# Performance work log

Measured on AMD Instinct MI355X. Metric: run time of the kernel, lower is better.

## Reference

```python
import jax, jax.numpy as jnp
import numpy as np

B, C, H = 128, 3, 224
PATCH_NUM, PS = 14, 16          # patch_size = image_size / patch_num
NP = PATCH_NUM * PATCH_NUM      # 196 patches
TOP_K = 20
D = 768                         # ViT-B hidden dim
NUM_CLASSES = 1000


def setup_inputs() -> dict:
    key = jax.random.key(0)
    k1, k2, k3, k4, k5 = jax.random.split(key, 5)
    return {
        "inputs": jax.random.normal(k1, (B, C, H, H), jnp.float32),
        "patch_grad": jax.random.normal(k2, (B, NP, D), jnp.float32),
        "attack_w": jax.random.uniform(k3, (C, H, H), jnp.float32),  # torch.rand init
        "w_cls": jax.random.normal(k4, (C * NP, NUM_CLASSES), jnp.float32) * 0.02,
        "targets": jax.random.randint(k5, (B,), 0, NUM_CLASSES),
    }


def reference(inputs, patch_grad, attack_w, w_cls, targets):
    # --- top-k patch selection from patch-embedding gradients ---
    # sum over batch, then over embedding dim -> [NP]
    sum_patch = patch_grad.sum(axis=0).sum(axis=1)
    _, top_idx = jax.lax.top_k(sum_patch, TOP_K)  # distinct patch indices

    # --- vectorized equivalent of the per-pixel double loop ---
    # patch (ix, iy) -> pixel block [ix*PS:(ix+1)*PS, iy*PS:(iy+1)*PS]
    ix = top_idx // PATCH_NUM
    iy = top_idx % PATCH_NUM
    mask_p = jnp.zeros((PATCH_NUM, PATCH_NUM), inputs.dtype).at[ix, iy].set(1.0)
    mask = jnp.kron(mask_p, jnp.ones((PS, PS), inputs.dtype))  # [H, H] pixel mask
    x = inputs + mask[None, None, :, :] * attack_w[None, :, :, :]  # [B,C,H,H]

    # --- surrogate classifier head (stand-in for aux_vit second forward) ---
    # per-patch average pool, flatten, linear -> logits [B, NUM_CLASSES]
    pooled = x.reshape(B, C, PATCH_NUM, PS, PATCH_NUM, PS).mean(axis=(3, 5))
    logits = pooled.reshape(B, -1) @ w_cls

    targets_prob = jax.nn.softmax(logits, axis=1)
    # original applies CrossEntropyLoss to the *probabilities* (treats them as logits)
    logp = jax.nn.log_softmax(targets_prob, axis=1)
    ce = -jnp.take_along_axis(logp, targets[:, None], axis=1)[:, 0]  # [B]

    u = 0.0
    l2loss = jnp.mean(attack_w * attack_w)
    loss = u * l2loss - (1.0 - u) * ce.mean()
    return targets_prob, loss
```

## Files before the change

kernel.cpp:

```cpp
#include <hip/hip_runtime.h>
#include <math.h>

#define PA_OFF    0
#define APOOL_OFF 2048
#define MA_OFF    3072
#define IPOOL_OFF 4096
#define PL_OFF    81920

__global__ __launch_bounds__(256) void k1_fused(
    const float* __restrict__ inputs,
    const float* __restrict__ patch_grad,
    const float* __restrict__ attack_w,
    float* __restrict__ ws)
{
  __shared__ __align__(16) float lds[448];
  const int bid = blockIdx.x;
  const int t   = threadIdx.x;

  if (bid < 2688) {
    const int img = bid / 7, pp = bid - img * 7;
    const float* src = inputs + (size_t)img * 50176 + (size_t)pp * 32 * 224;
    if (t < 224) {
      const int c4 = t % 56, rg = t / 56;
      float4 v[8];
      #pragma unroll
      for (int j = 0; j < 8; ++j) {
        const int row = (j >> 2) * 16 + (j & 3) * 4 + rg;
        v[j] = *(const float4*)(src + row * 224 + c4 * 4);
      }
      float s0 = 0.f, s1 = 0.f;
      #pragma unroll
      for (int j = 0; j < 4; ++j) s0 += (v[j].x + v[j].y) + (v[j].z + v[j].w);
      #pragma unroll
      for (int j = 4; j < 8; ++j) s1 += (v[j].x + v[j].y) + (v[j].z + v[j].w);
      lds[(0 * 4 + rg) * 56 + c4] = s0;
      lds[(1 * 4 + rg) * 56 + c4] = s1;
    }
    __syncthreads();
    if (t < 28) {
      const int pxl = t / 14, py = t - pxl * 14;
      float s = 0.f;
      #pragma unroll
      for (int rg = 0; rg < 4; ++rg)
        #pragma unroll
        for (int i4 = 0; i4 < 4; ++i4)
          s += lds[(pxl * 4 + rg) * 56 + py * 4 + i4];
      const int b = img / 3, c = img - b * 3;
      const int px = pp * 2 + pxl;
      ws[IPOOL_OFF + (size_t)b * 588 + c * 196 + px * 14 + py] = s * (1.f / 256.f);
    }
  } else if (bid < 4256) {
    const int a = bid - 2688;
    const int p = a >> 3, chunk = a & 7;
    const float* base = patch_grad + (size_t)chunk * 16 * 150528 + (size_t)p * 768;
    float4 v[12];
    #pragma unroll
    for (int j = 0; j < 12; ++j) {
      const int idx = j * 256 + t;
      const int r   = idx / 192;
      const int off = idx - r * 192;
      v[j] = *(const float4*)(base + (size_t)r * 150528 + off * 4);
    }
    float acc = 0.f;
    #pragma unroll
    for (int j = 0; j < 12; ++j) acc += (v[j].x + v[j].y) + (v[j].z + v[j].w);
    #pragma unroll
    for (int o = 32; o > 0; o >>= 1) acc += __shfl_down(acc, o, 64);
    if ((t & 63) == 0) lds[t >> 6] = acc;
    __syncthreads();
    if (t == 0) ws[PA_OFF + a] = lds[0] + lds[1] + lds[2] + lds[3];
  } else {
    const int a = bid - 4256;
    const int c = a / 14, px = a - c * 14;
    const float* img = attack_w + (size_t)c * 50176;
    if (t < 224) {
      const int c4 = t % 56, rg = t / 56;
      float4 v[4];
      #pragma unroll
      for (int jj = 0; jj < 4; ++jj) {
        const int row = px * 16 + jj * 4 + rg;
        v[jj] = *(const float4*)(img + row * 224 + c4 * 4);
      }
      float s = 0.f;
      #pragma unroll
      for (int jj = 0; jj < 4; ++jj) s += (v[jj].x + v[jj].y) + (v[jj].z + v[jj].w);
      lds[rg * 56 + c4] = s;
    }
    __syncthreads();
    if (t < 14) {
      float s = 0.f;
      #pragma unroll
      for (int rg = 0; rg < 4; ++rg)
        for (int i4 = 0; i4 < 4; ++i4)
          s += lds[rg * 56 + t * 4 + i4];
      ws[APOOL_OFF + c * 196 + px * 14 + t] = s * (1.f / 256.f);
    }
  }
}

__global__ __launch_bounds__(256) void k2_topk(float* __restrict__ ws,
                                               float* __restrict__ d_loss)
{
  __shared__ float sp[196];
  __shared__ float maskp[196];
  const int t = threadIdx.x;
  if (t < 196) {
    const float* pa = ws + PA_OFF;
    float s = 0.f;
    #pragma unroll
    for (int j = 0; j < 8; ++j) s += pa[t * 8 + j];
    sp[t] = s;
  }
  if (t == 0) *d_loss = 0.f;
  __syncthreads();
  if (t < 196) {
    const float v = sp[t];
    int cnt = 0;
    for (int j = 0; j < 196; ++j) {
      const float u = sp[j];
      cnt += (u > v || (u == v && j < t)) ? 1 : 0;
    }
    maskp[t] = (cnt < 20) ? 1.f : 0.f;
  }
  __syncthreads();
  for (int k = t; k < 588; k += 256) {
    const int p = k % 196;
    ws[MA_OFF + k] = maskp[p] * ws[APOOL_OFF + k];
  }
}

__global__ __launch_bounds__(256) void k3_gemm(const float* __restrict__ w_cls,
                                               float* __restrict__ ws)
{
  __shared__ __align__(16) float lp[147 * 8];
  const int bid = blockIdx.x;
  const int ks = bid & 3;
  const int nt = (bid >> 2) & 15;
  const int bg = bid >> 6;
  const int t  = threadIdx.x;
  const float* ipool = ws + IPOOL_OFF;
  const float* ma    = ws + MA_OFF;
  for (int idx = t; idx < 1176; idx += 256) {
    const int bb = idx / 147;
    const int kk = idx - bb * 147;
    const int k  = ks * 147 + kk;
    lp[kk * 8 + bb] = ipool[(size_t)(bg * 8 + bb) * 588 + k] + ma[k];
  }
  __syncthreads();
  const int lane = t & 63, g = t >> 6;
  const int n = nt * 64 + lane;
  const bool valid = n < 1000;
  float a0 = 0, a1 = 0;
  const float* wc = w_cls + (size_t)ks * 147 * 1000 + n;
  #pragma unroll 7
  for (int kk = 0; kk < 147; ++kk) {
    const float w = valid ? wc[(size_t)kk * 1000] : 0.f;
    const float2 pv = *(const float2*)&lp[kk * 8 + g * 2];
    a0 += pv.x * w; a1 += pv.y * w;
  }
  float* pl = ws + PL_OFF;
  const int rowb = ks * 128 + bg * 8 + g * 2;
  pl[(size_t)(rowb + 0) * 1024 + n] = a0;
  pl[(size_t)(rowb + 1) * 1024 + n] = a1;
}

__global__ __launch_bounds__(256) void k4_softmax(const float* __restrict__ ws,
                                                  const int* __restrict__ targets,
                                                  float* __restrict__ out)
{
  __shared__ float red[4];
  __shared__ float sh_pt;
  const int b = blockIdx.x, t = threadIdx.x;
  const float* pl = ws + PL_OFF;
  float l[4]; bool val[4];
  #pragma unroll
  for (int j = 0; j < 4; ++j) {
    const int n = j * 256 + t;
    val[j] = (n < 1000);
    float s = -INFINITY;
    if (val[j]) {
      s = 0.f;
      #pragma unroll
      for (int ks = 0; ks < 4; ++ks) s += pl[(size_t)(ks * 128 + b) * 1024 + n];
    }
    l[j] = s;
  }
  float m = fmaxf(fmaxf(l[0], l[1]), fmaxf(l[2], l[3]));
  #pragma unroll
  for (int o = 32; o > 0; o >>= 1) m = fmaxf(m, __shfl_down(m, o, 64));
  if ((t & 63) == 0) red[t >> 6] = m;
  __syncthreads();
  const float m1 = fmaxf(fmaxf(red[0], red[1]), fmaxf(red[2], red[3]));
  __syncthreads();
  float e[4]; float s = 0.f;
  #pragma unroll
  for (int j = 0; j < 4; ++j) { e[j] = val[j] ? expf(l[j] - m1) : 0.f; s += e[j]; }
  #pragma unroll
  for (int o = 32; o > 0; o >>= 1) s += __shfl_down(s, o, 64);
  if ((t & 63) == 0) red[t >> 6] = s;
  __syncthreads();
  const float S1 = red[0] + red[1] + red[2] + red[3];
  __syncthreads();
  const float inv = 1.f / S1;
  const int tgt = targets[b];
  float p[4];
  #pragma unroll
  for (int j = 0; j < 4; ++j) {
    const int n = j * 256 + t;
    if (val[j]) {
      p[j] = e[j] * inv;
      out[(size_t)b * 1000 + n] = p[j];
      if (n == tgt) sh_pt = p[j];
    } else {
      p[j] = -INFINITY;
    }
  }
  float m2 = fmaxf(fmaxf(p[0], p[1]), fmaxf(p[2], p[3]));
  #pragma unroll
  for (int o = 32; o > 0; o >>= 1) m2 = fmaxf(m2, __shfl_down(m2, o, 64));
  if ((t & 63) == 0) red[t >> 6] = m2;
  __syncthreads();
  const float M2 = fmaxf(fmaxf(red[0], red[1]), fmaxf(red[2], red[3]));
  __syncthreads();
  float s2 = 0.f;
  #pragma unroll
  for (int j = 0; j < 4; ++j) s2 += val[j] ? expf(p[j] - M2) : 0.f;
  #pragma unroll
  for (int o = 32; o > 0; o >>= 1) s2 += __shfl_down(s2, o, 64);
  if ((t & 63) == 0) red[t >> 6] = s2;
  __syncthreads();
  if (t == 0) {
    const float S2 = red[0] + red[1] + red[2] + red[3];
    const float lse2 = M2 + logf(S2);
    atomicAdd(out + 128000, (sh_pt - lse2) * (1.f / 128.f));
  }
}

extern "C" void kernel_launch(void* const* d_in, const int* in_sizes, int n_in,
                              void* d_out, int out_size, void* d_ws, size_t ws_size,
                              hipStream_t stream) {
  const float* inputs     = (const float*)d_in[0];
  const float* patch_grad = (const float*)d_in[1];
  const float* attack_w   = (const float*)d_in[2];
  const float* w_cls      = (const float*)d_in[3];
  const int*   targets    = (const int*)d_in[4];
  float* out = (float*)d_out;
  float* ws  = (float*)d_ws;

  hipLaunchKernelGGL(k1_fused,  dim3(4298), dim3(256), 0, stream,
                     inputs, patch_grad, attack_w, ws);
  hipLaunchKernelGGL(k2_topk,   dim3(1),    dim3(256), 0, stream, ws, out + 128000);
  hipLaunchKernelGGL(k3_gemm,   dim3(1024), dim3(256), 0, stream, w_cls, ws);
  hipLaunchKernelGGL(k4_softmax, dim3(128), dim3(256), 0, stream, ws, targets, out);
}
```

Baseline: 207.1 us.

## Split fused reduction kernel into wave-per-row pooling and contiguous patch-grad reduction

Splits the fused first-stage kernel into two kernels. The image and attack-weight pooling now uses one wavefront per 16-row patch strip, with shuffle reductions in place of LDS and block barriers. The patch-gradient reduction now has each wave read four contiguous 768-float rows and write per-(patch, batch) partials, so the top-k kernel sums 128 partials per patch. This is meant to make the patch_grad reads contiguous and drop barriers. The cost is an extra kernel launch, a larger partial buffer, and a longer serial sum in the single-block top-k kernel.

```diff
diff --git a/kernel.cpp b/kernel.cpp
--- a/kernel.cpp
+++ b/kernel.cpp
@@ -2,99 +2,90 @@
 #include <math.h>
 
 #define PA_OFF    0
-#define APOOL_OFF 2048
-#define MA_OFF    3072
-#define IPOOL_OFF 4096
-#define PL_OFF    81920
-
-__global__ __launch_bounds__(256) void k1_fused(
+#define APOOL_OFF 25600
+#define MA_OFF    26624
+#define IPOOL_OFF 28672
+#define PL_OFF    106496
+
+__global__ __launch_bounds__(256) void k1a_pool(
     const float* __restrict__ inputs,
-    const float* __restrict__ patch_grad,
     const float* __restrict__ attack_w,
     float* __restrict__ ws)
 {
-  __shared__ __align__(16) float lds[448];
-  const int bid = blockIdx.x;
-  const int t   = threadIdx.x;
-
-  if (bid < 2688) {
-    const int img = bid / 7, pp = bid - img * 7;
-    const float* src = inputs + (size_t)img * 50176 + (size_t)pp * 32 * 224;
-    if (t < 224) {
-      const int c4 = t % 56, rg = t / 56;
-      float4 v[8];
-      #pragma unroll
-      for (int j = 0; j < 8; ++j) {
-        const int row = (j >> 2) * 16 + (j & 3) * 4 + rg;
-        v[j] = *(const float4*)(src + row * 224 + c4 * 4);
-      }
-      float s0 = 0.f, s1 = 0.f;
-      #pragma unroll
-      for (int j = 0; j < 4; ++j) s0 += (v[j].x + v[j].y) + (v[j].z + v[j].w);
-      #pragma unroll
-      for (int j = 4; j < 8; ++j) s1 += (v[j].x + v[j].y) + (v[j].z + v[j].w);
-      lds[(0 * 4 + rg) * 56 + c4] = s0;
-      lds[(1 * 4 + rg) * 56 + c4] = s1;
-    }
-    __syncthreads();
-    if (t < 28) {
-      const int pxl = t / 14, py = t - pxl * 14;
-      float s = 0.f;
-      #pragma unroll
-      for (int rg = 0; rg < 4; ++rg)
-        #pragma unroll
-        for (int i4 = 0; i4 < 4; ++i4)
-          s += lds[(pxl * 4 + rg) * 56 + py * 4 + i4];
+  const int w    = blockIdx.x * 4 + (threadIdx.x >> 6);
+  const int lane = threadIdx.x & 63;
+  if (w >= 5418) return;
+  const int img = w / 14, px = w - img * 14;
+  const float* base = (img < 384)
+      ? inputs + (size_t)img * 50176
+      : attack_w + (size_t)(img - 384) * 50176;
+  const float* src = base + px * 3584;
+
+  float4 s = make_float4(0.f, 0.f, 0.f, 0.f);
+  if (lane < 56) {
+    float4 v[16];
+    #pragma unroll
+    for (int r = 0; r < 16; ++r)
+      v[r] = *(const float4*)(src + r * 224 + lane * 4);
+    #pragma unroll
+    for (int r = 0; r < 16; ++r) {
+      s.x += v[r].x; s.y += v[r].y; s.z += v[r].z; s.w += v[r].w;
+    }
+  }
+  s.x += __shfl_xor(s.x, 1); s.y += __shfl_xor(s.y, 1);
+  s.z += __shfl_xor(s.z, 1); s.w += __shfl_xor(s.w, 1);
+  s.x += __shfl_xor(s.x, 2); s.y += __shfl_xor(s.y, 2);
+  s.z += __shfl_xor(s.z, 2); s.w += __shfl_xor(s.w, 2);
+  if ((lane & 3) == 0 && lane < 56) {
+    const int py = lane >> 2;
+    const float ps = ((s.x + s.y) + (s.z + s.w)) * (1.f / 256.f);
+    if (img < 384) {
       const int b = img / 3, c = img - b * 3;
-      const int px = pp * 2 + pxl;
-      ws[IPOOL_OFF + (size_t)b * 588 + c * 196 + px * 14 + py] = s * (1.f / 256.f);
-    }
-  } else if (bid < 4256) {
-    const int a = bid - 2688;
-    const int p = a >> 3, chunk = a & 7;
-    const float* base = patch_grad + (size_t)chunk * 16 * 150528 + (size_t)p * 768;
-    float4 v[12];
-    #pragma unroll
-    for (int j = 0; j < 12; ++j) {
-      const int idx = j * 256 + t;
-      const int r   = idx / 192;
-      const int off = idx - r * 192;
-      v[j] = *(const float4*)(base + (size_t)r * 150528 + off * 4);
-    }
-    float acc = 0.f;
-    #pragma unroll
-    for (int j = 0; j < 12; ++j) acc += (v[j].x + v[j].y) + (v[j].z + v[j].w);
-    #pragma unroll
-    for (int o = 32; o > 0; o >>= 1) acc += __shfl_down(acc, o, 64);
-    if ((t & 63) == 0) lds[t >> 6] = acc;
-    __syncthreads();
-    if (t == 0) ws[PA_OFF + a] = lds[0] + lds[1] + lds[2] + lds[3];
-  } else {
-    const int a = bid - 4256;
-    const int c = a / 14, px = a - c * 14;
-    const float* img = attack_w + (size_t)c * 50176;
-    if (t < 224) {
-      const int c4 = t % 56, rg = t / 56;
-      float4 v[4];
-      #pragma unroll
-      for (int jj = 0; jj < 4; ++jj) {
-        const int row = px * 16 + jj * 4 + rg;
-        v[jj] = *(const float4*)(img + row * 224 + c4 * 4);
-      }
-      float s = 0.f;
-      #pragma unroll
-      for (int jj = 0; jj < 4; ++jj) s += (v[jj].x + v[jj].y) + (v[jj].z + v[jj].w);
-      lds[rg * 56 + c4] = s;
-    }
-    __syncthreads();
-    if (t < 14) {
-      float s = 0.f;
-      #pragma unroll
-      for (int rg = 0; rg < 4; ++rg)
-        for (int i4 = 0; i4 < 4; ++i4)
-          s += lds[rg * 56 + t * 4 + i4];
-      ws[APOOL_OFF + c * 196 + px * 14 + t] = s * (1.f / 256.f);
-    }
+      ws[IPOOL_OFF + (size_t)b * 588 + c * 196 + px * 14 + py] = ps;
+    } else {
+      ws[APOOL_OFF + (img - 384) * 196 + px * 14 + py] = ps;
+    }
+  }
+}
+
+__global__ __launch_bounds__(256) void k1b_pgrad(
+    const float* __restrict__ patch_grad,
+    float* __restrict__ ws)
+{
+  const int w    = blockIdx.x * 4 + (threadIdx.x >> 6);
+  const int lane = threadIdx.x & 63;
+  const int R0   = w * 4;
+  const float* base = patch_grad + (size_t)R0 * 768;
+
+  float4 v[12];
+  #pragma unroll
+  for (int j = 0; j < 12; ++j)
+    v[j] = *(const float4*)(base + (size_t)(lane + 64 * j) * 4);
+
+  float s0 = 0.f, s1 = 0.f, s2 = 0.f, s3 = 0.f;
+  #pragma unroll
+  for (int j = 0; j < 3; ++j)  s0 += (v[j].x + v[j].y) + (v[j].z + v[j].w);
+  #pragma unroll
+  for (int j = 3; j < 6; ++j)  s1 += (v[j].x + v[j].y) + (v[j].z + v[j].w);
+  #pragma unroll
+  for (int j = 6; j < 9; ++j)  s2 += (v[j].x + v[j].y) + (v[j].z + v[j].w);
+  #pragma unroll
+  for (int j = 9; j < 12; ++j) s3 += (v[j].x + v[j].y) + (v[j].z + v[j].w);
+
+  #pragma unroll
+  for (int o = 32; o > 0; o >>= 1) {
+    s0 += __shfl_down(s0, o, 64);
+    s1 += __shfl_down(s1, o, 64);
+    s2 += __shfl_down(s2, o, 64);
+    s3 += __shfl_down(s3, o, 64);
+  }
+  if (lane == 0) {
+    const int b = R0 / 196, p = R0 - b * 196;
+    float* pa = ws + PA_OFF;
+    pa[(p + 0) * 128 + b] = s0;
+    pa[(p + 1) * 128 + b] = s1;
+    pa[(p + 2) * 128 + b] = s2;
+    pa[(p + 3) * 128 + b] = s3;
   }
 }
 
@@ -105,11 +96,14 @@
   __shared__ float maskp[196];
   const int t = threadIdx.x;
   if (t < 196) {
-    const float* pa = ws + PA_OFF;
-    float s = 0.f;
+    const float4* q = (const float4*)(ws + PA_OFF + (size_t)t * 128);
+    float4 a = make_float4(0.f, 0.f, 0.f, 0.f);
     #pragma unroll
-    for (int j = 0; j < 8; ++j) s += pa[t * 8 + j];
-    sp[t] = s;
+    for (int j = 0; j < 32; ++j) {
+      const float4 v = q[j];
+      a.x += v.x; a.y += v.y; a.z += v.z; a.w += v.w;
+    }
+    sp[t] = (a.x + a.y) + (a.z + a.w);
   }
   if (t == 0) *d_loss = 0.f;
   __syncthreads();
@@ -247,8 +241,8 @@
   float* out = (float*)d_out;
   float* ws  = (float*)d_ws;
 
-  hipLaunchKernelGGL(k1_fused,  dim3(4298), dim3(256), 0, stream,
-                     inputs, patch_grad, attack_w, ws);
+  hipLaunchKernelGGL(k1a_pool,  dim3(1355), dim3(256), 0, stream, inputs, attack_w, ws);
+  hipLaunchKernelGGL(k1b_pgrad, dim3(1568), dim3(256), 0, stream, patch_grad, ws);
   hipLaunchKernelGGL(k2_topk,   dim3(1),    dim3(256), 0, stream, ws, out + 128000);
   hipLaunchKernelGGL(k3_gemm,   dim3(1024), dim3(256), 0, stream, w_cls, ws);
   hipLaunchKernelGGL(k4_softmax, dim3(128), dim3(256), 0, stream, ws, targets, out);
```

New measurement: 212.4 us. 2.5% more time.
